# Performance work log

Hardware: AMD Instinct MI355X
Metric: run time of the kernel (lower is better)

The kernel has to match this reference:

```python
import jax, jax.numpy as jnp
import numpy as np
from jax import lax

KSIZE = 3
SIGMA = 0.3 * ((KSIZE - 1) * 0.5 - 1) + 0.8  # cv2 auto-sigma for k=3 -> 0.8

def _gauss_kernel(k, sigma):
    ax = np.arange(k, dtype=np.float64) - (k - 1) / 2
    xx, yy = np.meshgrid(ax, ax, indexing='ij')
    ker = np.exp(-(xx ** 2 + yy ** 2) / (2.0 * sigma ** 2))
    ker /= ker.sum()
    return jnp.asarray(ker, jnp.float32)

SCHARR_X = jnp.array([[-3., 0., 3.], [-10., 0., 10.], [-3., 0., 3.]], jnp.float32)
SCHARR_Y = SCHARR_X.T  # cv2.Scharr(dy=1)

def _conv2d_reflect(img, ker):
    # img: [B,1,H,W]; cross-correlation (like cv2.filter2D) with BORDER_REFLECT_101
    p = ker.shape[0] // 2
    img = jnp.pad(img, ((0, 0), (0, 0), (p, p), (p, p)), mode='reflect')
    return lax.conv_general_dilated(img, ker[None, None], (1, 1), 'VALID')

def setup_inputs() -> dict:
    key = jax.random.key(0)
    x = jax.random.uniform(key, (8, 3, 1024, 1024), dtype=jnp.float32) * 255.0
    return {"x": x}

def reference(x):
    B, C, H, W = x.shape
    # cv2 RGB2GRAY weights
    rgb_w = jnp.array([0.299, 0.587, 0.114], dtype=x.dtype)
    gray = jnp.einsum('bchw,c->bhw', x, rgb_w)[:, None]  # [B,1,H,W]
    blurred = _conv2d_reflect(gray, _gauss_kernel(KSIZE, SIGMA))
    sx = _conv2d_reflect(blurred, SCHARR_X)
    sy = _conv2d_reflect(blurred, SCHARR_Y)
    mag = jnp.sqrt(sx * sx + sy * sy)  # L2_gradient=True
    # forward returns gradient magnitude replicated across channels
    return jnp.broadcast_to(mag, (B, C, H, W))
```

## Files before the change

### kernel.cpp

```cpp
#include <hip/hip_runtime.h>
#include <math.h>


#define IMG_H 1024
#define IMG_W 1024
#define TH 16
#define TW 128

#define GYR (TH + 4)
#define GXD (TW + 8)
#define GXS (GXD + 4)
#define BYR (TH + 2)
#define BXS (TW + 4)

#define GW0 0.52201125f
#define GW1 0.23899437f

__device__ __forceinline__ int reflect101(int v, int n) {
    v = (v < 0) ? -v : v;
    return (v >= n) ? (2 * n - 2 - v) : v;
}

__global__ __launch_bounds__(256)
void edge_kernel(const float* __restrict__ in, float* __restrict__ out, int B) {
    __shared__ float sg[GYR][GXS];
    __shared__ float sb[BYR][BXS];

    const int tid = threadIdx.x;
    const int x0 = blockIdx.x * TW;
    const int y0 = blockIdx.y * TH;
    const int b  = blockIdx.z;

    const size_t plane = (size_t)IMG_H * IMG_W;
    const float* pr = in + (size_t)b * 3 * plane;
    const float* pg = pr + plane;
    const float* pb = pg + plane;

    for (int i = tid; i < GYR * (GXD / 4); i += 256) {
        int gy  = i / (GXD / 4);
        int gx4 = (i - gy * (GXD / 4)) * 4;
        int y = reflect101(y0 - 2 + gy, IMG_H);
        int x = x0 - 4 + gx4;
        float4 r4, g4, b4;
        if ((unsigned)x <= (unsigned)(IMG_W - 4)) {
            size_t o = (size_t)y * IMG_W + x;
            r4 = *(const float4*)(pr + o);
            g4 = *(const float4*)(pg + o);
            b4 = *(const float4*)(pb + o);
        } else {
            int xe0 = reflect101(x,     IMG_W), xe1 = reflect101(x + 1, IMG_W);
            int xe2 = reflect101(x + 2, IMG_W), xe3 = reflect101(x + 3, IMG_W);
            size_t ro = (size_t)y * IMG_W;
            r4 = make_float4(pr[ro+xe0], pr[ro+xe1], pr[ro+xe2], pr[ro+xe3]);
            g4 = make_float4(pg[ro+xe0], pg[ro+xe1], pg[ro+xe2], pg[ro+xe3]);
            b4 = make_float4(pb[ro+xe0], pb[ro+xe1], pb[ro+xe2], pb[ro+xe3]);
        }
        float4 gr;
        gr.x = 0.299f * r4.x + 0.587f * g4.x + 0.114f * b4.x;
        gr.y = 0.299f * r4.y + 0.587f * g4.y + 0.114f * b4.y;
        gr.z = 0.299f * r4.z + 0.587f * g4.z + 0.114f * b4.z;
        gr.w = 0.299f * r4.w + 0.587f * g4.w + 0.114f * b4.w;
        *(float4*)&sg[gy][gx4] = gr;
    }
    __syncthreads();

    for (int i = tid; i < BYR * (BXS / 4); i += 256) {
        int by  = i / (BXS / 4);
        int bx4 = (i - by * (BXS / 4)) * 4;
        float4 r0a = *(const float4*)&sg[by    ][bx4];
        float4 r0b = *(const float4*)&sg[by    ][bx4 + 4];
        float4 r1a = *(const float4*)&sg[by + 1][bx4];
        float4 r1b = *(const float4*)&sg[by + 1][bx4 + 4];
        float4 r2a = *(const float4*)&sg[by + 2][bx4];
        float4 r2b = *(const float4*)&sg[by + 2][bx4 + 4];
        float v2 = GW1 * (r0a.z + r2a.z) + GW0 * r1a.z;
        float v3 = GW1 * (r0a.w + r2a.w) + GW0 * r1a.w;
        float v4 = GW1 * (r0b.x + r2b.x) + GW0 * r1b.x;
        float v5 = GW1 * (r0b.y + r2b.y) + GW0 * r1b.y;
        float v6 = GW1 * (r0b.z + r2b.z) + GW0 * r1b.z;
        float v7 = GW1 * (r0b.w + r2b.w) + GW0 * r1b.w;
        float4 o;
        o.x = GW1 * (v2 + v4) + GW0 * v3;
        o.y = GW1 * (v3 + v5) + GW0 * v4;
        o.z = GW1 * (v4 + v6) + GW0 * v5;
        o.w = GW1 * (v5 + v7) + GW0 * v6;
        *(float4*)&sb[by][bx4] = o;
    }
    __syncthreads();

    const int c4 = (tid & 31) * 4;
    const int ty_base = tid >> 5;
    float* po = out + (size_t)b * 3 * plane;
    for (int ty = ty_base; ty < TH; ty += 8) {
        float4 t0a = *(const float4*)&sb[ty    ][c4];
        float4 t0b = *(const float4*)&sb[ty    ][c4 + 4];
        float4 t1a = *(const float4*)&sb[ty + 1][c4];
        float4 t1b = *(const float4*)&sb[ty + 1][c4 + 4];
        float4 t2a = *(const float4*)&sb[ty + 2][c4];
        float4 t2b = *(const float4*)&sb[ty + 2][c4 + 4];
        float r0[6] = {t0a.x, t0a.y, t0a.z, t0a.w, t0b.x, t0b.y};
        float r1[6] = {t1a.x, t1a.y, t1a.z, t1a.w, t1b.x, t1b.y};
        float r2[6] = {t2a.x, t2a.y, t2a.z, t2a.w, t2b.x, t2b.y};
        float4 mag;
        float* mp = &mag.x;
        #pragma unroll
        for (int k = 0; k < 4; ++k) {
            float sx = 3.0f * (r0[k+2] - r0[k]) + 10.0f * (r1[k+2] - r1[k]) + 3.0f * (r2[k+2] - r2[k]);
            float sy = 3.0f * (r2[k]   - r0[k]) + 10.0f * (r2[k+1] - r0[k+1]) + 3.0f * (r2[k+2] - r0[k+2]);
            mp[k] = sqrtf(sx * sx + sy * sy);
        }
        size_t o = (size_t)(y0 + ty) * IMG_W + (x0 + c4);
        *(float4*)(po + o)             = mag;
        *(float4*)(po + o + plane)     = mag;
        *(float4*)(po + o + 2 * plane) = mag;
    }
}

extern "C" void kernel_launch(void* const* d_in, const int* in_sizes, int n_in,
                              void* d_out, int out_size, void* d_ws, size_t ws_size,
                              hipStream_t stream) {
    const float* in = (const float*)d_in[0];
    float* out = (float*)d_out;
    const int B = in_sizes[0] / (3 * IMG_H * IMG_W);
    dim3 grid(IMG_W / TW, IMG_H / TH, B);
    edge_kernel<<<grid, dim3(256), 0, stream>>>(in, out, B);
}
```

Measured before the change: 182.9 us.

## Fold blur into separable 5-tap Scharr filters and use register-sliding rows

Composes the Gaussian blur with the Scharr kernels into separable 5-tap smoothing and difference filters, removing the intermediate blurred shared-memory tile and its extra barrier. Each thread now computes four consecutive output rows with a rolling 5-row register window of horizontal partial results. The tile height doubles to 32 and all global loads are issued into registers before the grayscale conversion, which raises the memory-level parallelism. In exchange, register pressure rises, and because the blur output is no longer computed separately, border handling could differ slightly from the reference's reflect padding of the blurred image.

```diff
diff --git a/kernel.cpp b/kernel.cpp
--- a/kernel.cpp
+++ b/kernel.cpp
@@ -4,17 +4,18 @@
 
 #define IMG_H 1024
 #define IMG_W 1024
-#define TH 16
+#define TH 32
 #define TW 128
+#define GYR (TH + 4)
+#define GXD 136
+#define NIT ((GYR * (GXD/4) + 255) / 256)
+#define NITEMS (GYR * (GXD/4))
 
-#define GYR (TH + 4)
-#define GXD (TW + 8)
-#define GXS (GXD + 4)
-#define BYR (TH + 2)
-#define BXS (TW + 4)
-
-#define GW0 0.52201125f
-#define GW1 0.23899437f
+#define W0 0.52201125f
+#define W1 0.23899437f
+#define AV0 0.71698311f
+#define AV1 3.95597745f
+#define AV2 6.65407872f
 
 __device__ __forceinline__ int reflect101(int v, int n) {
     v = (v < 0) ? -v : v;
@@ -23,8 +24,7 @@
 
 __global__ __launch_bounds__(256)
 void edge_kernel(const float* __restrict__ in, float* __restrict__ out, int B) {
-    __shared__ float sg[GYR][GXS];
-    __shared__ float sb[BYR][BXS];
+    __shared__ float sg[GYR][GXD];
 
     const int tid = threadIdx.x;
     const int x0 = blockIdx.x * TW;
@@ -36,80 +36,84 @@
     const float* pg = pr + plane;
     const float* pb = pg + plane;
 
-    for (int i = tid; i < GYR * (GXD / 4); i += 256) {
-        int gy  = i / (GXD / 4);
-        int gx4 = (i - gy * (GXD / 4)) * 4;
-        int y = reflect101(y0 - 2 + gy, IMG_H);
-        int x = x0 - 4 + gx4;
-        float4 r4, g4, b4;
-        if ((unsigned)x <= (unsigned)(IMG_W - 4)) {
-            size_t o = (size_t)y * IMG_W + x;
-            r4 = *(const float4*)(pr + o);
-            g4 = *(const float4*)(pg + o);
-            b4 = *(const float4*)(pb + o);
-        } else {
-            int xe0 = reflect101(x,     IMG_W), xe1 = reflect101(x + 1, IMG_W);
-            int xe2 = reflect101(x + 2, IMG_W), xe3 = reflect101(x + 3, IMG_W);
-            size_t ro = (size_t)y * IMG_W;
-            r4 = make_float4(pr[ro+xe0], pr[ro+xe1], pr[ro+xe2], pr[ro+xe3]);
-            g4 = make_float4(pg[ro+xe0], pg[ro+xe1], pg[ro+xe2], pg[ro+xe3]);
-            b4 = make_float4(pb[ro+xe0], pb[ro+xe1], pb[ro+xe2], pb[ro+xe3]);
+    float4 R[NIT], G[NIT], Bv[NIT];
+    #pragma unroll
+    for (int it = 0; it < NIT; ++it) {
+        int i = tid + it * 256;
+        if (i < NITEMS) {
+            int gy  = i / (GXD / 4);
+            int gx4 = (i - gy * (GXD / 4)) * 4;
+            int y = reflect101(y0 - 2 + gy, IMG_H);
+            int x = x0 - 4 + gx4;
+            if ((unsigned)x <= (unsigned)(IMG_W - 4)) {
+                size_t o = (size_t)y * IMG_W + x;
+                R[it]  = *(const float4*)(pr + o);
+                G[it]  = *(const float4*)(pg + o);
+                Bv[it] = *(const float4*)(pb + o);
+            } else {
+                int xe0 = reflect101(x,     IMG_W), xe1 = reflect101(x + 1, IMG_W);
+                int xe2 = reflect101(x + 2, IMG_W), xe3 = reflect101(x + 3, IMG_W);
+                size_t ro = (size_t)y * IMG_W;
+                R[it]  = make_float4(pr[ro+xe0], pr[ro+xe1], pr[ro+xe2], pr[ro+xe3]);
+                G[it]  = make_float4(pg[ro+xe0], pg[ro+xe1], pg[ro+xe2], pg[ro+xe3]);
+                Bv[it] = make_float4(pb[ro+xe0], pb[ro+xe1], pb[ro+xe2], pb[ro+xe3]);
+            }
         }
-        float4 gr;
-        gr.x = 0.299f * r4.x + 0.587f * g4.x + 0.114f * b4.x;
-        gr.y = 0.299f * r4.y + 0.587f * g4.y + 0.114f * b4.y;
-        gr.z = 0.299f * r4.z + 0.587f * g4.z + 0.114f * b4.z;
-        gr.w = 0.299f * r4.w + 0.587f * g4.w + 0.114f * b4.w;
-        *(float4*)&sg[gy][gx4] = gr;
+    }
+    #pragma unroll
+    for (int it = 0; it < NIT; ++it) {
+        int i = tid + it * 256;
+        if (i < NITEMS) {
+            int gy  = i / (GXD / 4);
+            int gx4 = (i - gy * (GXD / 4)) * 4;
+            float4 gr;
+            gr.x = 0.299f * R[it].x + 0.587f * G[it].x + 0.114f * Bv[it].x;
+            gr.y = 0.299f * R[it].y + 0.587f * G[it].y + 0.114f * Bv[it].y;
+            gr.z = 0.299f * R[it].z + 0.587f * G[it].z + 0.114f * Bv[it].z;
+            gr.w = 0.299f * R[it].w + 0.587f * G[it].w + 0.114f * Bv[it].w;
+            *(float4*)&sg[gy][gx4] = gr;
+        }
     }
     __syncthreads();
 
-    for (int i = tid; i < BYR * (BXS / 4); i += 256) {
-        int by  = i / (BXS / 4);
-        int bx4 = (i - by * (BXS / 4)) * 4;
-        float4 r0a = *(const float4*)&sg[by    ][bx4];
-        float4 r0b = *(const float4*)&sg[by    ][bx4 + 4];
-        float4 r1a = *(const float4*)&sg[by + 1][bx4];
-        float4 r1b = *(const float4*)&sg[by + 1][bx4 + 4];
-        float4 r2a = *(const float4*)&sg[by + 2][bx4];
-        float4 r2b = *(const float4*)&sg[by + 2][bx4 + 4];
-        float v2 = GW1 * (r0a.z + r2a.z) + GW0 * r1a.z;
-        float v3 = GW1 * (r0a.w + r2a.w) + GW0 * r1a.w;
-        float v4 = GW1 * (r0b.x + r2b.x) + GW0 * r1b.x;
-        float v5 = GW1 * (r0b.y + r2b.y) + GW0 * r1b.y;
-        float v6 = GW1 * (r0b.z + r2b.z) + GW0 * r1b.z;
-        float v7 = GW1 * (r0b.w + r2b.w) + GW0 * r1b.w;
-        float4 o;
-        o.x = GW1 * (v2 + v4) + GW0 * v3;
-        o.y = GW1 * (v3 + v5) + GW0 * v4;
-        o.z = GW1 * (v4 + v6) + GW0 * v5;
-        o.w = GW1 * (v5 + v7) + GW0 * v6;
-        *(float4*)&sb[by][bx4] = o;
-    }
-    __syncthreads();
+    const int tx  = tid & 31;
+    const int tyg = tid >> 5;
+    const int c4  = tx * 4;
+    const int r0  = tyg * 4;
 
-    const int c4 = (tid & 31) * 4;
-    const int ty_base = tid >> 5;
+    float hs[5][4], hd[5][4];
+
+    auto hrow = [&](int rr, float* HS, float* HD) {
+        const float* row = &sg[rr][c4];
+        float4 ga = *(const float4*)(row);
+        float4 gb = *(const float4*)(row + 4);
+        float4 gc = *(const float4*)(row + 8);
+        float g[12] = {ga.x, ga.y, ga.z, ga.w, gb.x, gb.y, gb.z, gb.w,
+                       gc.x, gc.y, gc.z, gc.w};
+        #pragma unroll
+        for (int k = 0; k < 4; ++k) {
+            HS[k] = AV0 * (g[k+2] + g[k+6]) + AV1 * (g[k+3] + g[k+5]) + AV2 * g[k+4];
+            HD[k] = W1 * (g[k+6] - g[k+2]) + W0 * (g[k+5] - g[k+3]);
+        }
+    };
+
+    #pragma unroll
+    for (int s = 0; s < 5; ++s) hrow(r0 + s, hs[s], hd[s]);
+
     float* po = out + (size_t)b * 3 * plane;
-    for (int ty = ty_base; ty < TH; ty += 8) {
-        float4 t0a = *(const float4*)&sb[ty    ][c4];
-        float4 t0b = *(const float4*)&sb[ty    ][c4 + 4];
-        float4 t1a = *(const float4*)&sb[ty + 1][c4];
-        float4 t1b = *(const float4*)&sb[ty + 1][c4 + 4];
-        float4 t2a = *(const float4*)&sb[ty + 2][c4];
-        float4 t2b = *(const float4*)&sb[ty + 2][c4 + 4];
-        float r0[6] = {t0a.x, t0a.y, t0a.z, t0a.w, t0b.x, t0b.y};
-        float r1[6] = {t1a.x, t1a.y, t1a.z, t1a.w, t1b.x, t1b.y};
-        float r2[6] = {t2a.x, t2a.y, t2a.z, t2a.w, t2b.x, t2b.y};
+    #pragma unroll
+    for (int t = 0; t < 4; ++t) {
+        if (t > 0) hrow(r0 + 4 + t, hs[(t + 4) % 5], hd[(t + 4) % 5]);
+        const int i0 = t % 5, i1 = (t+1) % 5, i2 = (t+2) % 5, i3 = (t+3) % 5, i4 = (t+4) % 5;
         float4 mag;
         float* mp = &mag.x;
         #pragma unroll
         for (int k = 0; k < 4; ++k) {
-            float sx = 3.0f * (r0[k+2] - r0[k]) + 10.0f * (r1[k+2] - r1[k]) + 3.0f * (r2[k+2] - r2[k]);
-            float sy = 3.0f * (r2[k]   - r0[k]) + 10.0f * (r2[k+1] - r0[k+1]) + 3.0f * (r2[k+2] - r0[k+2]);
+            float sx = AV0 * (hd[i0][k] + hd[i4][k]) + AV1 * (hd[i1][k] + hd[i3][k]) + AV2 * hd[i2][k];
+            float sy = W1 * (hs[i4][k] - hs[i0][k]) + W0 * (hs[i3][k] - hs[i1][k]);
             mp[k] = sqrtf(sx * sx + sy * sy);
         }
-        size_t o = (size_t)(y0 + ty) * IMG_W + (x0 + c4);
+        size_t o = (size_t)(y0 + r0 + t) * IMG_W + (x0 + c4);
         *(float4*)(po + o)             = mag;
         *(float4*)(po + o + plane)     = mag;
         *(float4*)(po + o + 2 * plane) = mag;
```

New measurement: 178.4 us. 1.03x faster.
